# Kernel tuning notes

Hardware: AMD Instinct MI355X
Metric: run time of the kernel (lower is better)

## Reference

```python
import jax, jax.numpy as jnp
import numpy as np

GROUPS = 32
EPS = 1e-5


def group_norm(x, gamma, beta):
    B, C, D, H, W = x.shape
    xr = x.reshape(B, GROUPS, C // GROUPS, D, H, W)
    mean = xr.mean(axis=(2, 3, 4, 5), keepdims=True)
    var = xr.var(axis=(2, 3, 4, 5), keepdims=True)
    xn = (xr - mean) * jax.lax.rsqrt(var + EPS)
    xn = xn.reshape(B, C, D, H, W)
    return xn * gamma[None, :, None, None, None] + beta[None, :, None, None, None]


def conv1x1(h, w, b):
    # 1x1x1 Conv3d == channel matmul. w: [O, C], b: [O]
    return jnp.einsum('oc,bcdhw->bodhw', w, h) + b[None, :, None, None, None]


def setup_inputs() -> dict:
    key = jax.random.key(0)
    ks = jax.random.split(key, 10)
    B, C, D, H, W = 2, 128, 16, 16, 16
    x = jax.random.normal(ks[0], (B, C, D, H, W), dtype=jnp.float32)
    gn_w = jnp.ones((C,), dtype=jnp.float32)
    gn_b = jnp.zeros((C,), dtype=jnp.float32)
    # xavier_uniform for [C, C, 1, 1, 1] conv: fan_in = fan_out = C
    lim = float(np.sqrt(6.0 / (C + C)))
    wq = jax.random.uniform(ks[1], (C, C), jnp.float32, -lim, lim)
    wk = jax.random.uniform(ks[2], (C, C), jnp.float32, -lim, lim)
    wv = jax.random.uniform(ks[3], (C, C), jnp.float32, -lim, lim)
    wp = jax.random.uniform(ks[4], (C, C), jnp.float32, -lim, lim) * 1e-05
    bq = jnp.zeros((C,), jnp.float32)
    bk = jnp.zeros((C,), jnp.float32)
    bv = jnp.zeros((C,), jnp.float32)
    bp = jnp.zeros((C,), jnp.float32)
    return {"x": x, "gn_w": gn_w, "gn_b": gn_b, "wq": wq, "bq": bq,
            "wk": wk, "bk": bk, "wv": wv, "bv": bv, "wp": wp, "bp": bp}


def reference(x, gn_w, gn_b, wq, bq, wk, bk, wv, bv, wp, bp):
    B, C, D, H, W = x.shape
    N = D * H * W
    h = group_norm(x, gn_w, gn_b)
    q = conv1x1(h, wq, bq)
    k = conv1x1(h, wk, bk)
    v = conv1x1(h, wv, bv)
    q = q.transpose(0, 2, 3, 4, 1).reshape(B, N, C)   # [B, N, C]
    k = k.reshape(B, C, N)                            # [B, C, N]
    v = v.transpose(0, 2, 3, 4, 1).reshape(B, N, C)   # [B, N, C]
    w = jnp.einsum('bnc,bcm->bnm', q, k) * (C ** -0.5)  # [B, N, N]
    w = jax.nn.softmax(w, axis=-1)
    h = jnp.einsum('bnm,bmc->bnc', w, v)              # [B, N, C]
    h = h.reshape(B, D, H, W, C).transpose(0, 4, 1, 2, 3)
    h = conv1x1(h, wp, bp)
    return x + h
```

## Files before the change

### kernel.cpp

```cpp
#include <hip/hip_runtime.h>
#include <math.h>

#define CC 128
#define NN 4096
#define BB 2
#define NGROUPS 32
#define CPG 4
#define GSIZE (CPG*NN)
#define KSPLIT 8

typedef __attribute__((ext_vector_type(8))) __bf16 bf16x8;
typedef __attribute__((ext_vector_type(4))) float floatx4;

__device__ __forceinline__ unsigned short f2bf(float f) {
  union { float f; unsigned u; } v; v.f = f;
  unsigned r = v.u + 0x7fff + ((v.u >> 16) & 1);
  return (unsigned short)(r >> 16);
}
__device__ __forceinline__ float bf2f(unsigned short u) {
  return __uint_as_float(((unsigned)u) << 16);
}


__device__ __forceinline__ void stage_tile(const unsigned short* __restrict__ gtile,
                                           unsigned short* ltile, int w, int lane) {
  #pragma unroll
  for (int j = 0; j < 4; j++) {
    int off = (w*4 + j) * 512;
    __builtin_amdgcn_global_load_lds(
        (const __attribute__((address_space(1))) unsigned int*)(gtile + off + lane*8),
        (__attribute__((address_space(3))) unsigned int*)(ltile + off),
        16, 0, 0);
  }
}

__global__ void gn_stats_kernel(const float* __restrict__ x, float2* __restrict__ stats,
                                const float* __restrict__ wq, const float* __restrict__ wk,
                                const float* __restrict__ wv, const float* __restrict__ wp,
                                unsigned short* __restrict__ wqb, unsigned short* __restrict__ wkb,
                                unsigned short* __restrict__ wvb, unsigned short* __restrict__ wpb) {
  int t = threadIdx.x;
  if (blockIdx.x < 256) {
    int bid = blockIdx.x;
    const float4* base = (const float4*)(x + (size_t)bid * 4096);
    float4 v = base[t];
    float s  = v.x + v.y + v.z + v.w;
    float ss = v.x*v.x + v.y*v.y + v.z*v.z + v.w*v.w;
    #pragma unroll
    for (int off = 1; off < 64; off <<= 1) {
      s  += __shfl_xor(s, off);
      ss += __shfl_xor(ss, off);
    }
    __shared__ float sred[4], ssred[4];
    if ((t & 63) == 0) { sred[t >> 6] = s; ssred[t >> 6] = ss; }
    __syncthreads();
    if (t == 0)
      stats[bid] = make_float2(sred[0]+sred[1]+sred[2]+sred[3],
                               ssred[0]+ssred[1]+ssred[2]+ssred[3]);
  } else {
    const float sc = 0.08838834764831845f;
    int i = (blockIdx.x - 256) * 256 + t;
    int id = i >> 12, local = i & 4095;
    const float* src = id==0 ? wq : id==1 ? wk : id==2 ? wv : wp;
    unsigned short* dst = id==0 ? wqb : id==1 ? wkb : id==2 ? wvb : wpb;
    float s = (id == 0) ? sc : 1.0f;
    float4 v = ((const float4*)src)[local];
    unsigned p0 = (unsigned)f2bf(v.x*s) | ((unsigned)f2bf(v.y*s) << 16);
    unsigned p1 = (unsigned)f2bf(v.z*s) | ((unsigned)f2bf(v.w*s) << 16);
    ((uint2*)dst)[local] = make_uint2(p0, p1);
  }
}

__global__ __launch_bounds__(256, 2) void qkv_kernel(
    const float* __restrict__ x, const float2* __restrict__ stats,
    const float* __restrict__ gamma, const float* __restrict__ beta,
    const unsigned short* __restrict__ wqb, const unsigned short* __restrict__ wkb,
    const unsigned short* __restrict__ wvb,
    const float* __restrict__ bq, const float* __restrict__ bk, const float* __restrict__ bv,
    unsigned short* __restrict__ q, unsigned short* __restrict__ k, unsigned short* __restrict__ v) {
  int b = blockIdx.y, n0 = blockIdx.x * 16;
  __shared__ unsigned short hs[16][130];
  __shared__ unsigned short vs[16][136];
  __shared__ float gm[NGROUPS], gr[NGROUPS], aa[CC], ab[CC];
  int t = threadIdx.x;
  if (t < NGROUPS) {
    float su = 0.f, ssq = 0.f;
    #pragma unroll
    for (int j = 0; j < 4; j++) {
      float2 p = stats[(b*NGROUPS + t)*4 + j];
      su += p.x; ssq += p.y;
    }
    float mean = su * (1.0f/GSIZE);
    float var  = ssq * (1.0f/GSIZE) - mean*mean;
    gm[t] = mean;
    gr[t] = rsqrtf(var + 1e-5f);
  }
  __syncthreads();
  if (t < CC) {
    int g = t >> 2;
    float a = gr[g] * gamma[t];
    aa[t] = a;
    ab[t] = beta[t] - gm[g] * a;
  }
  __syncthreads();
  #pragma unroll
  for (int j = 0; j < 2; j++) {
    int idx = j*256 + t;
    int c = idx >> 2, n4 = idx & 3;
    float4 xv = *(const float4*)(x + ((size_t)b*CC + c)*NN + n0 + n4*4);
    float a = aa[c], bc = ab[c];
    hs[n4*4+0][c] = f2bf(a*xv.x + bc);
    hs[n4*4+1][c] = f2bf(a*xv.y + bc);
    hs[n4*4+2][c] = f2bf(a*xv.z + bc);
    hs[n4*4+3][c] = f2bf(a*xv.w + bc);
  }
  __syncthreads();
  int w = t >> 6, lane = t & 63, quad = lane >> 4, c = lane & 15;
  int o0 = w * 32;
  bf16x8 af[4];
  #pragma unroll
  for (int ks = 0; ks < 4; ks++)
    af[ks] = *(const bf16x8*)&hs[c][ks*32 + quad*8];
  floatx4 aq[2], ak[2], av[2];
  #pragma unroll
  for (int ct = 0; ct < 2; ct++) {
    aq[ct] = (floatx4){0.f,0.f,0.f,0.f};
    ak[ct] = (floatx4){0.f,0.f,0.f,0.f};
    av[ct] = (floatx4){0.f,0.f,0.f,0.f};
  }
  #pragma unroll
  for (int ks = 0; ks < 4; ks++) {
    #pragma unroll
    for (int ct = 0; ct < 2; ct++) {
      size_t woff = (size_t)(o0 + ct*16 + c)*CC + ks*32 + quad*8;
      bf16x8 bq8 = *(const bf16x8*)(wqb + woff);
      bf16x8 bk8 = *(const bf16x8*)(wkb + woff);
      bf16x8 bv8 = *(const bf16x8*)(wvb + woff);
      aq[ct] = __builtin_amdgcn_mfma_f32_16x16x32_bf16(af[ks], bq8, aq[ct], 0, 0, 0);
      ak[ct] = __builtin_amdgcn_mfma_f32_16x16x32_bf16(af[ks], bk8, ak[ct], 0, 0, 0);
      av[ct] = __builtin_amdgcn_mfma_f32_16x16x32_bf16(af[ks], bv8, av[ct], 0, 0, 0);
    }
  }
  {
    const float sc = 0.08838834764831845f;
    size_t base = (size_t)b*NN*CC + (size_t)blockIdx.x*2048 + w*512;
    #pragma unroll
    for (int ct = 0; ct < 2; ct++) {
      float bqi = bq[o0 + ct*16 + c] * sc;
      float bki = bk[o0 + ct*16 + c];
      #pragma unroll
      for (int r = 0; r < 4; r++) {
        int idx = (quad*4 + r)*32 + ct*16 + c;
        q[base + idx] = f2bf(aq[ct][r] + bqi);
        k[base + idx] = f2bf(ak[ct][r] + bki);
      }
    }
  }
  #pragma unroll
  for (int ct = 0; ct < 2; ct++) {
    float bvi = bv[o0 + ct*16 + c];
    #pragma unroll
    for (int r = 0; r < 4; r++)
      vs[quad*4 + r][o0 + ct*16 + c] = f2bf(av[ct][r] + bvi);
  }
  __syncthreads();
  {
    int ch = t >> 1, part = t & 1;
    int mbase = (n0 & 16) + part*8;
    unsigned pk[4];
    #pragma unroll
    for (int j = 0; j < 4; j++) {
      unsigned lo = vs[part*8 + j*2    ][ch];
      unsigned hi = vs[part*8 + j*2 + 1][ch];
      pk[j] = lo | (hi << 16);
    }
    *(uint4*)(v + (size_t)b*NN*CC + ((size_t)(n0 >> 5))*4096 + (ch >> 4)*512
              + (ch & 15)*32 + mbase) = make_uint4(pk[0], pk[1], pk[2], pk[3]);
  }
}

__global__ __launch_bounds__(256, 2) void attn_kernel(
    const unsigned short* __restrict__ qm,
    const unsigned short* __restrict__ km,
    const unsigned short* __restrict__ vm,
    unsigned short* __restrict__ Opart,
    float* __restrict__ lpart) {
  int b    = blockIdx.z;
  int kh   = blockIdx.y;
  int t    = threadIdx.x;
  int w    = t >> 6, lane = t & 63, quad = lane >> 4, c = lane & 15;

  __shared__ unsigned short Kbuf[2][8192];
  __shared__ unsigned short Vbuf[8192];
  __shared__ unsigned short Pl[4][32][72];

  int fragoff = c*32 + quad*8;

  bf16x8 qa[2][4];
  const unsigned short* qbase = qm + (size_t)b*NN*CC + ((size_t)(blockIdx.x*8 + w*2))*2048;
  #pragma unroll
  for (int rt = 0; rt < 2; rt++)
    #pragma unroll
    for (int ks = 0; ks < 4; ks++)
      qa[rt][ks] = *(const bf16x8*)(qbase + rt*2048 + ks*512 + fragoff);

  floatx4 O[2][8];
  #pragma unroll
  for (int rt = 0; rt < 2; rt++)
    #pragma unroll
    for (int ct = 0; ct < 8; ct++) O[rt][ct] = (floatx4){0.f,0.f,0.f,0.f};
  float lsum[2][4];
  #pragma unroll
  for (int rt = 0; rt < 2; rt++)
    #pragma unroll
    for (int r = 0; r < 4; r++) lsum[rt][r] = 0.f;

  const unsigned short* kt0 = km + (size_t)b*NN*CC + (size_t)kh*(NN/KSPLIT)*CC;
  const unsigned short* vt0 = vm + (size_t)b*NN*CC + (size_t)kh*(NN/KSPLIT)*CC;

  const int ITERS = NN/KSPLIT/64;

  stage_tile(kt0, Kbuf[0], w, lane);
  stage_tile(vt0, Vbuf, w, lane);
  __syncthreads();

  for (int it = 0; it < ITERS; it++) {
    if (it+1 < ITERS) stage_tile(kt0 + (size_t)(it+1)*8192, Kbuf[(it+1)&1], w, lane);
    const unsigned short* Kcur = Kbuf[it&1];
    floatx4 S[2][4];
    #pragma unroll
    for (int rt = 0; rt < 2; rt++)
      #pragma unroll
      for (int ct = 0; ct < 4; ct++) S[rt][ct] = (floatx4){0.f,0.f,0.f,0.f};
    #pragma unroll
    for (int ks = 0; ks < 4; ks++) {
      #pragma unroll
      for (int ct = 0; ct < 4; ct++) {
        bf16x8 kf = *(const bf16x8*)&Kcur[ct*2048 + ks*512 + fragoff];
        S[0][ct] = __builtin_amdgcn_mfma_f32_16x16x32_bf16(qa[0][ks], kf, S[0][ct], 0, 0, 0);
        S[1][ct] = __builtin_amdgcn_mfma_f32_16x16x32_bf16(qa[1][ks], kf, S[1][ct], 0, 0, 0);
      }
    }
    #pragma unroll
    for (int rt = 0; rt < 2; rt++) {
      #pragma unroll
      for (int ct = 0; ct < 4; ct++) {
        float e0 = __expf(S[rt][ct][0]);
        float e1 = __expf(S[rt][ct][1]);
        float e2 = __expf(S[rt][ct][2]);
        float e3 = __expf(S[rt][ct][3]);
        lsum[rt][0] += e0; lsum[rt][1] += e1;
        lsum[rt][2] += e2; lsum[rt][3] += e3;
        bool odd = (c & 1);
        float s01 = odd ? e0 : e1;
        float g01 = __shfl_xor(s01, 1);
        unsigned lo0 = __float_as_uint(odd ? g01 : e0);
        unsigned hi0 = __float_as_uint(odd ? e1 : g01);
        unsigned p0 = (hi0 & 0xffff0000u) | (lo0 >> 16);
        float s23 = odd ? e2 : e3;
        float g23 = __shfl_xor(s23, 1);
        unsigned lo1 = __float_as_uint(odd ? g23 : e2);
        unsigned hi1 = __float_as_uint(odd ? e3 : g23);
        unsigned p1 = (hi1 & 0xffff0000u) | (lo1 >> 16);
        int colpair = ct*16 + (c & ~1);
        int rowA = rt*16 + quad*4 + (odd ? 1 : 0);
        int rowB = rt*16 + quad*4 + (odd ? 3 : 2);
        *(unsigned*)&Pl[w][rowA][colpair] = p0;
        *(unsigned*)&Pl[w][rowB][colpair] = p1;
      }
    }
    __syncthreads();
    #pragma unroll
    for (int ks2 = 0; ks2 < 2; ks2++) {
      bf16x8 pa0 = *(const bf16x8*)(&Pl[w][c     ][ks2*32 + quad*8]);
      bf16x8 pa1 = *(const bf16x8*)(&Pl[w][16 + c][ks2*32 + quad*8]);
      #pragma unroll
      for (int ct = 0; ct < 8; ct++) {
        bf16x8 vf = *(const bf16x8*)&Vbuf[ks2*4096 + ct*512 + fragoff];
        O[0][ct] = __builtin_amdgcn_mfma_f32_16x16x32_bf16(pa0, vf, O[0][ct], 0, 0, 0);
        O[1][ct] = __builtin_amdgcn_mfma_f32_16x16x32_bf16(pa1, vf, O[1][ct], 0, 0, 0);
      }
    }
    __syncthreads();
    if (it+1 < ITERS) stage_tile(vt0 + (size_t)(it+1)*8192, Vbuf, w, lane);
  }

  size_t nbase = (size_t)(kh*BB + b)*NN + blockIdx.x*128 + w*32;
  #pragma unroll
  for (int rt = 0; rt < 2; rt++)
    #pragma unroll
    for (int r = 0; r < 4; r++) {
      float vsum = lsum[rt][r];
      vsum += __shfl_xor(vsum, 1);
      vsum += __shfl_xor(vsum, 2);
      vsum += __shfl_xor(vsum, 4);
      vsum += __shfl_xor(vsum, 8);
      if (c == 0) lpart[nbase + rt*16 + quad*4 + r] = vsum;
    }
  bool odd = (c & 1);
  int colpair = (c & ~1);
  #pragma unroll
  for (int rt = 0; rt < 2; rt++) {
    #pragma unroll
    for (int ct = 0; ct < 8; ct++) {
      unsigned u0 = f2bf(O[rt][ct][0]);
      unsigned u1 = f2bf(O[rt][ct][1]);
      unsigned u2 = f2bf(O[rt][ct][2]);
      unsigned u3 = f2bf(O[rt][ct][3]);
      unsigned s01 = odd ? u0 : u1;
      unsigned g01 = __shfl_xor((int)s01, 1);
      unsigned p0 = odd ? (g01 | (u1 << 16)) : (u0 | (g01 << 16));
      unsigned s23 = odd ? u2 : u3;
      unsigned g23 = __shfl_xor((int)s23, 1);
      unsigned p1 = odd ? (g23 | (u3 << 16)) : (u2 | (g23 << 16));
      int rowA = rt*16 + quad*4 + (odd ? 1 : 0);
      int rowB = rt*16 + quad*4 + (odd ? 3 : 2);
      *(unsigned*)(Opart + (nbase + rowA)*CC + ct*16 + colpair) = p0;
      *(unsigned*)(Opart + (nbase + rowB)*CC + ct*16 + colpair) = p1;
    }
  }
}

__global__ __launch_bounds__(256, 2) void combine_kernel(
    const unsigned short* __restrict__ Opart, const float* __restrict__ lpart,
    const unsigned short* __restrict__ wpb, const float* __restrict__ bp,
    const float* __restrict__ x, float* __restrict__ out) {
  int b = blockIdx.y, n0 = blockIdx.x * 16;
  int t = threadIdx.x;
  __shared__ unsigned short hs[16][130];
  __shared__ float ps[16][132];
  __shared__ float linv[16];
  if (t < 16) {
    float l = 0.f;
    #pragma unroll
    for (int kh = 0; kh < KSPLIT; kh++)
      l += lpart[((size_t)(kh*BB + b))*NN + n0 + t];
    linv[t] = 1.f / l;
  }
  __syncthreads();
  {
    int n = t >> 4, ch0 = (t & 15) * 8;
    float acc[8];
    #pragma unroll
    for (int j = 0; j < 8; j++) acc[j] = 0.f;
    #pragma unroll
    for (int kh = 0; kh < KSPLIT; kh++) {
      uint4 a = *(const uint4*)(Opart + ((size_t)(kh*BB + b)*NN + n0 + n)*CC + ch0);
      unsigned uu[4] = {a.x, a.y, a.z, a.w};
      #pragma unroll
      for (int j = 0; j < 4; j++) {
        acc[j*2    ] += bf2f((unsigned short)(uu[j] & 0xffff));
        acc[j*2 + 1] += bf2f((unsigned short)(uu[j] >> 16));
      }
    }
    float li = linv[n];
    #pragma unroll
    for (int j = 0; j < 8; j++) hs[n][ch0 + j] = f2bf(acc[j] * li);
  }
  __syncthreads();
  int w = t >> 6, lane = t & 63, quad = lane >> 4, c = lane & 15;
  int o0 = w * 32;
  floatx4 acc[2];
  #pragma unroll
  for (int ct = 0; ct < 2; ct++) acc[ct] = (floatx4){0.f,0.f,0.f,0.f};
  #pragma unroll
  for (int ks = 0; ks < 4; ks++) {
    bf16x8 af = *(const bf16x8*)&hs[c][ks*32 + quad*8];
    #pragma unroll
    for (int ct = 0; ct < 2; ct++) {
      bf16x8 bfr = *(const bf16x8*)(wpb + (size_t)(o0 + ct*16 + c)*CC + ks*32 + quad*8);
      acc[ct] = __builtin_amdgcn_mfma_f32_16x16x32_bf16(af, bfr, acc[ct], 0, 0, 0);
    }
  }
  #pragma unroll
  for (int ct = 0; ct < 2; ct++)
    #pragma unroll
    for (int r = 0; r < 4; r++)
      ps[quad*4 + r][o0 + ct*16 + c] = acc[ct][r];
  __syncthreads();
  int o = t >> 1, nh = (t & 1) * 8;
  float bi = bp[o];
  const float* xr = x + ((size_t)b*CC + o)*NN + n0 + nh;
  float* orow = out + ((size_t)b*CC + o)*NN + n0 + nh;
  #pragma unroll
  for (int j4 = 0; j4 < 2; j4++) {
    float4 xv = ((const float4*)xr)[j4];
    float4 ov;
    ov.x = xv.x + ps[nh + j4*4 + 0][o] + bi;
    ov.y = xv.y + ps[nh + j4*4 + 1][o] + bi;
    ov.z = xv.z + ps[nh + j4*4 + 2][o] + bi;
    ov.w = xv.w + ps[nh + j4*4 + 3][o] + bi;
    ((float4*)orow)[j4] = ov;
  }
}

extern "C" void kernel_launch(void* const* d_in, const int* in_sizes, int n_in,
                              void* d_out, int out_size, void* d_ws, size_t ws_size,
                              hipStream_t stream) {
  const float* x    = (const float*)d_in[0];
  const float* gn_w = (const float*)d_in[1];
  const float* gn_b = (const float*)d_in[2];
  const float* wq   = (const float*)d_in[3];
  const float* bq   = (const float*)d_in[4];
  const float* wk   = (const float*)d_in[5];
  const float* bk   = (const float*)d_in[6];
  const float* wv   = (const float*)d_in[7];
  const float* bv   = (const float*)d_in[8];
  const float* wp   = (const float*)d_in[9];
  const float* bp   = (const float*)d_in[10];
  float* out = (float*)d_out;

  char* ws = (char*)d_ws;
  float2*         stats = (float2*)(ws);
  unsigned short* wqb   = (unsigned short*)(ws + 8192);
  unsigned short* wkb   = (unsigned short*)(ws + 8192 + 32768);
  unsigned short* wvb   = (unsigned short*)(ws + 8192 + 65536);
  unsigned short* wpb   = (unsigned short*)(ws + 8192 + 98304);
  unsigned short* qb    = (unsigned short*)(ws + 262144);
  unsigned short* kb    = (unsigned short*)(ws + 262144 + 2097152);
  unsigned short* vb    = (unsigned short*)(ws + 262144 + 2*2097152);
  unsigned short* Opart = (unsigned short*)(ws + 6553600);
  float*          lpart = (float*)(ws + 6553600 + 16777216);

  gn_stats_kernel<<<dim3(320), 256, 0, stream>>>(x, stats, wq, wk, wv, wp,
                                                 wqb, wkb, wvb, wpb);
  qkv_kernel     <<<dim3(NN/16, BB), 256, 0, stream>>>(x, stats, gn_w, gn_b,
                                                       wqb, wkb, wvb, bq, bk, bv,
                                                       qb, kb, vb);
  attn_kernel    <<<dim3(NN/128, KSPLIT, BB), 256, 0, stream>>>(qb, kb, vb, Opart, lpart);
  combine_kernel <<<dim3(NN/16, BB), 256, 0, stream>>>(Opart, lpart, wpb, bp, x, out);
}
```

Before: 121.8 us.

## Compute transposed QK scores to drop shuffles and single-buffer K tile

Swaps the MFMA operands so each lane holds four consecutive key columns of one query row. The exp values can then be packed to bf16 and written to the P tile with a single 8-byte store, with no cross-lane shuffles. Row sums collapse to one accumulator per row tile, and the final reduction needs two shuffles instead of four per row. The K tile is now single-buffered, with the next tile staged after the barrier instead of prefetched during the score compute. This cuts LDS and may raise occupancy, but it exposes more K load latency.

```diff
diff --git a/kernel.cpp b/kernel.cpp
--- a/kernel.cpp
+++ b/kernel.cpp
@@ -190,7 +190,7 @@
   int t    = threadIdx.x;
   int w    = t >> 6, lane = t & 63, quad = lane >> 4, c = lane & 15;
 
-  __shared__ unsigned short Kbuf[2][8192];
+  __shared__ unsigned short Kbuf[8192];
   __shared__ unsigned short Vbuf[8192];
   __shared__ unsigned short Pl[4][32][72];
 
@@ -209,67 +209,48 @@
   for (int rt = 0; rt < 2; rt++)
     #pragma unroll
     for (int ct = 0; ct < 8; ct++) O[rt][ct] = (floatx4){0.f,0.f,0.f,0.f};
-  float lsum[2][4];
-  #pragma unroll
-  for (int rt = 0; rt < 2; rt++)
-    #pragma unroll
-    for (int r = 0; r < 4; r++) lsum[rt][r] = 0.f;
+  float lsum[2] = {0.f, 0.f};
 
   const unsigned short* kt0 = km + (size_t)b*NN*CC + (size_t)kh*(NN/KSPLIT)*CC;
   const unsigned short* vt0 = vm + (size_t)b*NN*CC + (size_t)kh*(NN/KSPLIT)*CC;
 
   const int ITERS = NN/KSPLIT/64;
 
-  stage_tile(kt0, Kbuf[0], w, lane);
+  stage_tile(kt0, Kbuf, w, lane);
   stage_tile(vt0, Vbuf, w, lane);
   __syncthreads();
 
   for (int it = 0; it < ITERS; it++) {
-    if (it+1 < ITERS) stage_tile(kt0 + (size_t)(it+1)*8192, Kbuf[(it+1)&1], w, lane);
-    const unsigned short* Kcur = Kbuf[it&1];
-    floatx4 S[2][4];
+    floatx4 ST[2][4];
     #pragma unroll
     for (int rt = 0; rt < 2; rt++)
       #pragma unroll
-      for (int ct = 0; ct < 4; ct++) S[rt][ct] = (floatx4){0.f,0.f,0.f,0.f};
+      for (int ct = 0; ct < 4; ct++) ST[rt][ct] = (floatx4){0.f,0.f,0.f,0.f};
     #pragma unroll
     for (int ks = 0; ks < 4; ks++) {
       #pragma unroll
       for (int ct = 0; ct < 4; ct++) {
-        bf16x8 kf = *(const bf16x8*)&Kcur[ct*2048 + ks*512 + fragoff];
-        S[0][ct] = __builtin_amdgcn_mfma_f32_16x16x32_bf16(qa[0][ks], kf, S[0][ct], 0, 0, 0);
-        S[1][ct] = __builtin_amdgcn_mfma_f32_16x16x32_bf16(qa[1][ks], kf, S[1][ct], 0, 0, 0);
+        bf16x8 kf = *(const bf16x8*)&Kbuf[ct*2048 + ks*512 + fragoff];
+        ST[0][ct] = __builtin_amdgcn_mfma_f32_16x16x32_bf16(kf, qa[0][ks], ST[0][ct], 0, 0, 0);
+        ST[1][ct] = __builtin_amdgcn_mfma_f32_16x16x32_bf16(kf, qa[1][ks], ST[1][ct], 0, 0, 0);
       }
     }
     #pragma unroll
     for (int rt = 0; rt < 2; rt++) {
       #pragma unroll
       for (int ct = 0; ct < 4; ct++) {
-        float e0 = __expf(S[rt][ct][0]);
-        float e1 = __expf(S[rt][ct][1]);
-        float e2 = __expf(S[rt][ct][2]);
-        float e3 = __expf(S[rt][ct][3]);
-        lsum[rt][0] += e0; lsum[rt][1] += e1;
-        lsum[rt][2] += e2; lsum[rt][3] += e3;
-        bool odd = (c & 1);
-        float s01 = odd ? e0 : e1;
-        float g01 = __shfl_xor(s01, 1);
-        unsigned lo0 = __float_as_uint(odd ? g01 : e0);
-        unsigned hi0 = __float_as_uint(odd ? e1 : g01);
-        unsigned p0 = (hi0 & 0xffff0000u) | (lo0 >> 16);
-        float s23 = odd ? e2 : e3;
-        float g23 = __shfl_xor(s23, 1);
-        unsigned lo1 = __float_as_uint(odd ? g23 : e2);
-        unsigned hi1 = __float_as_uint(odd ? e3 : g23);
-        unsigned p1 = (hi1 & 0xffff0000u) | (lo1 >> 16);
-        int colpair = ct*16 + (c & ~1);
-        int rowA = rt*16 + quad*4 + (odd ? 1 : 0);
-        int rowB = rt*16 + quad*4 + (odd ? 3 : 2);
-        *(unsigned*)&Pl[w][rowA][colpair] = p0;
-        *(unsigned*)&Pl[w][rowB][colpair] = p1;
+        float e0 = __expf(ST[rt][ct][0]);
+        float e1 = __expf(ST[rt][ct][1]);
+        float e2 = __expf(ST[rt][ct][2]);
+        float e3 = __expf(ST[rt][ct][3]);
+        lsum[rt] += (e0 + e1) + (e2 + e3);
+        unsigned p01 = (__float_as_uint(e1) & 0xffff0000u) | (__float_as_uint(e0) >> 16);
+        unsigned p23 = (__float_as_uint(e3) & 0xffff0000u) | (__float_as_uint(e2) >> 16);
+        *(uint2*)&Pl[w][rt*16 + c][ct*16 + quad*4] = make_uint2(p01, p23);
       }
     }
     __syncthreads();
+    if (it+1 < ITERS) stage_tile(kt0 + (size_t)(it+1)*8192, Kbuf, w, lane);
     #pragma unroll
     for (int ks2 = 0; ks2 < 2; ks2++) {
       bf16x8 pa0 = *(const bf16x8*)(&Pl[w][c     ][ks2*32 + quad*8]);
@@ -287,16 +268,12 @@
 
   size_t nbase = (size_t)(kh*BB + b)*NN + blockIdx.x*128 + w*32;
   #pragma unroll
-  for (int rt = 0; rt < 2; rt++)
-    #pragma unroll
-    for (int r = 0; r < 4; r++) {
-      float vsum = lsum[rt][r];
-      vsum += __shfl_xor(vsum, 1);
-      vsum += __shfl_xor(vsum, 2);
-      vsum += __shfl_xor(vsum, 4);
-      vsum += __shfl_xor(vsum, 8);
-      if (c == 0) lpart[nbase + rt*16 + quad*4 + r] = vsum;
-    }
+  for (int rt = 0; rt < 2; rt++) {
+    float vsum = lsum[rt];
+    vsum += __shfl_xor(vsum, 16);
+    vsum += __shfl_xor(vsum, 32);
+    if (lane < 16) lpart[nbase + rt*16 + lane] = vsum;
+  }
   bool odd = (c & 1);
   int colpair = (c & ~1);
   #pragma unroll
```

Result: faster. 116.9 us, median of 2 (-4.1%).
